# Kernel tuning notes

Hardware: AMD Instinct MI355X
Metric: run time of the kernel (lower is better)

Reference implementation:

```python
import jax, jax.numpy as jnp
import numpy as np

N_NODES = 200000
D = 128            # in_channels
B_GRAPHS = 512     # batch_size
STEPS = 3          # processing_steps


def setup_inputs() -> dict:
    key = jax.random.key(0)
    k = jax.random.split(key, 6)
    x = jax.random.normal(k[0], (N_NODES, D), dtype=jnp.float32)
    batch = jnp.sort(jax.random.randint(k[1], (N_NODES,), 0, B_GRAPHS, dtype=jnp.int64))
    s = 0.1
    W_ih = jax.random.normal(k[2], (3 * D, 2 * D), dtype=jnp.float32) * s
    W_hh = jax.random.normal(k[3], (3 * D, D), dtype=jnp.float32) * s
    b_ih = jax.random.normal(k[4], (3 * D,), dtype=jnp.float32) * s
    b_hh = jax.random.normal(k[5], (3 * D,), dtype=jnp.float32) * s
    return {"x": x, "batch": batch, "batch_size": B_GRAPHS,
            "W_ih": W_ih, "W_hh": W_hh, "b_ih": b_ih, "b_hh": b_hh}


def _gru_cell(inp, h, W_ih, W_hh, b_ih, b_hh):
    # inp: [B, 2d], h: [B, d]; PyTorch GRU gate order: r, z, n
    gi = inp @ W_ih.T + b_ih  # [B, 3d]
    gh = h @ W_hh.T + b_hh    # [B, 3d]
    gi_r, gi_z, gi_n = jnp.split(gi, 3, axis=-1)
    gh_r, gh_z, gh_n = jnp.split(gh, 3, axis=-1)
    r = jax.nn.sigmoid(gi_r + gh_r)
    z = jax.nn.sigmoid(gi_z + gh_z)
    n = jnp.tanh(gi_n + r * gh_n)
    return (1.0 - z) * n + z * h


def reference(x, batch, batch_size, W_ih, W_hh, b_ih, b_hh):
    B = batch_size
    d = x.shape[1]
    h = jnp.zeros((B, d), dtype=x.dtype)
    q_star = jnp.zeros((B, 2 * d), dtype=x.dtype)
    for _ in range(STEPS):
        h = _gru_cell(q_star, h, W_ih, W_hh, b_ih, b_hh)
        q = h  # num_layers=1: output == new hidden state
        e = jnp.sum(x * q[batch], axis=-1)  # [N]
        m = jax.ops.segment_max(e, batch, num_segments=B)
        ex = jnp.exp(e - m[batch])
        s = jax.ops.segment_sum(ex, batch, num_segments=B)
        a = ex / (s[batch] + 1e-16)  # segment softmax weights [N]
        r = jax.ops.segment_sum(a[:, None] * x, batch, num_segments=B)  # [B, d]
        q_star = jnp.concatenate([q, r], axis=-1)
    return q_star
```

## Files before the change

### kernel.cpp

```cpp
#include <hip/hip_runtime.h>
#include <math.h>

constexpr int D = 128;
constexpr int B = 512;
constexpr int STEPS = 3;
constexpr int NW_IH = 3 * D * 2 * D;
constexpr int NW_HH = 3 * D * D;

__device__ __forceinline__ float sigmoidf_(float x) { return 1.f / (1.f + __expf(-x)); }
__device__ __forceinline__ float bflo(unsigned int u) { return __uint_as_float(u << 16); }
__device__ __forceinline__ float bfhi(unsigned int u) { return __uint_as_float(u & 0xffff0000u); }
__device__ __forceinline__ unsigned short f2bf_rn(float f) {
    unsigned int u = __float_as_uint(f);
    u += 0x7fffu + ((u >> 16) & 1u);
    return (unsigned short)(u >> 16);
}

__global__ __launch_bounds__(256) void k_prep(const float* __restrict__ Wih,
        const float* __restrict__ Whh, const int* __restrict__ batch, int n,
        unsigned short* __restrict__ wih_bf, unsigned short* __restrict__ whh_bf,
        int* __restrict__ seg) {
    int i = blockIdx.x * blockDim.x + threadIdx.x;
    if (i < NW_IH) wih_bf[i] = f2bf_rn(Wih[i]);
    else if (i < NW_IH + NW_HH) whh_bf[i - NW_IH] = f2bf_rn(Whh[i - NW_IH]);
    if (i <= B) {
        int lo = 0, hi = n;
        while (lo < hi) { int mid = (lo + hi) >> 1; if (batch[mid] < i) lo = mid + 1; else hi = mid; }
        seg[i] = lo;
    }
}

__global__ __launch_bounds__(1024, 8) void k_set2set(
        const float* __restrict__ x,
        const unsigned short* __restrict__ wih_bf,
        const unsigned short* __restrict__ whh_bf,
        const float* __restrict__ bih, const float* __restrict__ bhh,
        const int* __restrict__ seg, float* __restrict__ out) {
    __shared__ __align__(16) float s_q[2 * D];
    __shared__ __align__(16) float s_h[D];
    __shared__ float s_gi[3 * D], s_gh[3 * D];
    __shared__ float sm[64], sl[64];
    __shared__ __align__(16) float rpart[16][D];

    const int b = blockIdx.x;
    const int tid = threadIdx.x;
    const int start = seg[b], end = seg[b + 1];
    const int g = tid >> 4;
    const int s = tid & 15;

    if (tid < 2 * D) s_q[tid] = 0.f;
    if (tid < D) s_h[tid] = 0.f;
    __syncthreads();

    for (int step = 0; step < STEPS; ++step) {
        if (tid < 768) {
            const int row  = tid >> 1;
            const int half = tid & 1;
            float gi = half ? 0.f : bih[row];
            float gh = half ? bhh[row] : 0.f;
            const float4* q4 = (const float4*)s_q;
            const float4* h4 = (const float4*)s_h;
            const uint4* wr = (const uint4*)(wih_bf + (size_t)row * (2 * D)) + half * 16;
#pragma unroll 4
            for (int c = 0; c < 16; ++c) {
                uint4 w = wr[c];
                float4 qa = q4[half * 32 + c * 2];
                float4 qb = q4[half * 32 + c * 2 + 1];
                gi = fmaf(bflo(w.x), qa.x, gi); gi = fmaf(bfhi(w.x), qa.y, gi);
                gi = fmaf(bflo(w.y), qa.z, gi); gi = fmaf(bfhi(w.y), qa.w, gi);
                gi = fmaf(bflo(w.z), qb.x, gi); gi = fmaf(bfhi(w.z), qb.y, gi);
                gi = fmaf(bflo(w.w), qb.z, gi); gi = fmaf(bfhi(w.w), qb.w, gi);
            }
            const uint4* vr = (const uint4*)(whh_bf + (size_t)row * D) + half * 8;
#pragma unroll 4
            for (int c = 0; c < 8; ++c) {
                uint4 w = vr[c];
                float4 ha = h4[half * 16 + c * 2];
                float4 hb = h4[half * 16 + c * 2 + 1];
                gh = fmaf(bflo(w.x), ha.x, gh); gh = fmaf(bfhi(w.x), ha.y, gh);
                gh = fmaf(bflo(w.y), ha.z, gh); gh = fmaf(bfhi(w.y), ha.w, gh);
                gh = fmaf(bflo(w.z), hb.x, gh); gh = fmaf(bfhi(w.z), hb.y, gh);
                gh = fmaf(bflo(w.w), hb.z, gh); gh = fmaf(bfhi(w.w), hb.w, gh);
            }
            gi += __shfl_xor(gi, 1, 64);
            gh += __shfl_xor(gh, 1, 64);
            if (!half) { s_gi[row] = gi; s_gh[row] = gh; }
        }
        __syncthreads();
        if (tid < D) {
            const int t = tid;
            float r  = sigmoidf_(s_gi[t] + s_gh[t]);
            float z  = sigmoidf_(s_gi[D + t] + s_gh[D + t]);
            float nn = tanhf(s_gi[2 * D + t] + r * s_gh[2 * D + t]);
            float hn = (1.f - z) * nn + z * s_h[t];
            s_h[t] = hn;
            s_q[t] = hn;
        }
        __syncthreads();

        const float4 q0 = ((const float4*)s_h)[s * 2];
        const float4 q1 = ((const float4*)s_h)[s * 2 + 1];
        float m_run = -INFINITY, l_run = 0.f;
        float4 acc0 = {0.f, 0.f, 0.f, 0.f};
        float4 acc1 = {0.f, 0.f, 0.f, 0.f};

        auto process = [&](const float4& v0, const float4& v1) {
            float p;
            p = v0.x * q0.x;
            p = fmaf(v0.y, q0.y, p); p = fmaf(v0.z, q0.z, p); p = fmaf(v0.w, q0.w, p);
            p = fmaf(v1.x, q1.x, p); p = fmaf(v1.y, q1.y, p);
            p = fmaf(v1.z, q1.z, p); p = fmaf(v1.w, q1.w, p);
            p += __shfl_xor(p, 1, 64);
            p += __shfl_xor(p, 2, 64);
            p += __shfl_xor(p, 4, 64);
            p += __shfl_xor(p, 8, 64);
            float nm = fmaxf(m_run, p);
            float sc = __expf(m_run - nm);
            float a  = __expf(p - nm);
            l_run = fmaf(l_run, sc, a);
            acc0.x = fmaf(acc0.x, sc, a * v0.x);
            acc0.y = fmaf(acc0.y, sc, a * v0.y);
            acc0.z = fmaf(acc0.z, sc, a * v0.z);
            acc0.w = fmaf(acc0.w, sc, a * v0.w);
            acc1.x = fmaf(acc1.x, sc, a * v1.x);
            acc1.y = fmaf(acc1.y, sc, a * v1.y);
            acc1.z = fmaf(acc1.z, sc, a * v1.z);
            acc1.w = fmaf(acc1.w, sc, a * v1.w);
            m_run = nm;
        };

        for (int n0 = start + g; n0 < end; n0 += 128) {
            const int n1 = n0 + 64;
            const float* p0 = x + (size_t)n0 * D + s * 8;
            float4 a0 = *(const float4*)p0;
            float4 a1 = *(const float4*)(p0 + 4);
            if (n1 < end) {
                const float* p1 = x + (size_t)n1 * D + s * 8;
                float4 b0 = *(const float4*)p1;
                float4 b1 = *(const float4*)(p1 + 4);
                process(a0, a1);
                process(b0, b1);
            } else {
                process(a0, a1);
            }
        }

        if (s == 0) { sm[g] = m_run; sl[g] = l_run; }
        __syncthreads();

        {
            const float mv = sm[tid & 63];
            const float lv = sl[tid & 63];
            float M = mv;
            M = fmaxf(M, __shfl_xor(M, 1, 64));
            M = fmaxf(M, __shfl_xor(M, 2, 64));
            M = fmaxf(M, __shfl_xor(M, 4, 64));
            M = fmaxf(M, __shfl_xor(M, 8, 64));
            M = fmaxf(M, __shfl_xor(M, 16, 64));
            M = fmaxf(M, __shfl_xor(M, 32, 64));
            float term = (mv == -INFINITY) ? 0.f : lv * __expf(mv - M);
            term += __shfl_xor(term, 1, 64);
            term += __shfl_xor(term, 2, 64);
            term += __shfl_xor(term, 4, 64);
            term += __shfl_xor(term, 8, 64);
            term += __shfl_xor(term, 16, 64);
            term += __shfl_xor(term, 32, 64);
            const float inv = 1.f / (term + 1e-16f);
            const float fac = (m_run == -INFINITY) ? 0.f : __expf(m_run - M) * inv;
            acc0.x *= fac; acc0.y *= fac; acc0.z *= fac; acc0.w *= fac;
            acc1.x *= fac; acc1.y *= fac; acc1.z *= fac; acc1.w *= fac;
        }
        acc0.x += __shfl_xor(acc0.x, 16, 64); acc0.y += __shfl_xor(acc0.y, 16, 64);
        acc0.z += __shfl_xor(acc0.z, 16, 64); acc0.w += __shfl_xor(acc0.w, 16, 64);
        acc1.x += __shfl_xor(acc1.x, 16, 64); acc1.y += __shfl_xor(acc1.y, 16, 64);
        acc1.z += __shfl_xor(acc1.z, 16, 64); acc1.w += __shfl_xor(acc1.w, 16, 64);
        acc0.x += __shfl_xor(acc0.x, 32, 64); acc0.y += __shfl_xor(acc0.y, 32, 64);
        acc0.z += __shfl_xor(acc0.z, 32, 64); acc0.w += __shfl_xor(acc0.w, 32, 64);
        acc1.x += __shfl_xor(acc1.x, 32, 64); acc1.y += __shfl_xor(acc1.y, 32, 64);
        acc1.z += __shfl_xor(acc1.z, 32, 64); acc1.w += __shfl_xor(acc1.w, 32, 64);

        const int wv = tid >> 6;
        if ((tid & 63) < 16) {
            float4* dst = (float4*)&rpart[wv][s * 8];
            dst[0] = acc0; dst[1] = acc1;
        }
        __syncthreads();
        if (tid < D) {
            float v = 0.f;
#pragma unroll
            for (int w = 0; w < 16; ++w) v += rpart[w][tid];
            s_q[D + tid] = v;
        }
        __syncthreads();
    }

    if (tid < 2 * D) out[(size_t)b * (2 * D) + tid] = s_q[tid];
}

extern "C" void kernel_launch(void* const* d_in, const int* in_sizes, int n_in,
                              void* d_out, int out_size, void* d_ws, size_t ws_size,
                              hipStream_t stream) {
    const float* x    = (const float*)d_in[0];
    const int*   batch= (const int*)d_in[1];
    const float* Wih  = (const float*)d_in[3];
    const float* Whh  = (const float*)d_in[4];
    const float* bih  = (const float*)d_in[5];
    const float* bhh  = (const float*)d_in[6];
    const int n = in_sizes[0] / D;

    char* ws = (char*)d_ws;
    int* seg = (int*)ws;
    unsigned short* wih_bf = (unsigned short*)(ws + 4096);
    unsigned short* whh_bf = (unsigned short*)(ws + 4096 + (size_t)NW_IH * 2);

    const int total = NW_IH + NW_HH;
    k_prep<<<(total + 255) / 256, 256, 0, stream>>>(Wih, Whh, batch, n, wih_bf, whh_bf, seg);
    k_set2set<<<B, 1024, 0, stream>>>(x, wih_bf, whh_bf, bih, bhh, seg, (float*)d_out);
}
```

Measured before the change: 259.5 us.

## Shrink set2set blocks to 256 threads with double-buffered 4-node batches

Cuts each graph's block from 1024 to 256 threads, so each 16-lane group handles four nodes per iteration. Node rows are loaded into register buffers one batch ahead, and the first batch is issued before the GRU matvec so the load overlaps it. The online softmax rescale is amortised across four nodes, and each GRU thread now computes two full rows with no shuffle. The cost is fewer threads per graph, more registers per thread, and a longer serial GRU phase per thread.

```diff
diff --git a/kernel.cpp b/kernel.cpp
--- a/kernel.cpp
+++ b/kernel.cpp
@@ -15,6 +15,7 @@
     u += 0x7fffu + ((u >> 16) & 1u);
     return (unsigned short)(u >> 16);
 }
+__device__ __forceinline__ float4 ld4(const float* p) { return *(const float4*)p; }
 
 __global__ __launch_bounds__(256) void k_prep(const float* __restrict__ Wih,
         const float* __restrict__ Whh, const int* __restrict__ batch, int n,
@@ -30,7 +31,9 @@
     }
 }
 
-__global__ __launch_bounds__(1024, 8) void k_set2set(
+struct Trip { float4 a0, a1, b0, b1, c0, c1, d0, d1; };
+
+__global__ __launch_bounds__(256, 2) void k_set2set(
         const float* __restrict__ x,
         const unsigned short* __restrict__ wih_bf,
         const unsigned short* __restrict__ whh_bf,
@@ -39,8 +42,8 @@
     __shared__ __align__(16) float s_q[2 * D];
     __shared__ __align__(16) float s_h[D];
     __shared__ float s_gi[3 * D], s_gh[3 * D];
-    __shared__ float sm[64], sl[64];
-    __shared__ __align__(16) float rpart[16][D];
+    __shared__ float sm[16], sl[16];
+    __shared__ __align__(16) float rpart[4][D];
 
     const int b = blockIdx.x;
     const int tid = threadIdx.x;
@@ -52,39 +55,120 @@
     if (tid < D) s_h[tid] = 0.f;
     __syncthreads();
 
+    const int len = end - start;
+    const int F = len >> 6;
+    const float* xb = x + (size_t)(start + g) * D + s * 8;
+
+    float m_run, l_run;
+    float4 acc0, acc1;
+    float4 q0, q1;
+
+    auto load_trip = [&](Trip& T, int t) {
+        const float* p = xb + (size_t)t * (64 * D);
+        T.a0 = ld4(p);            T.a1 = ld4(p + 4);
+        T.b0 = ld4(p + 16 * D);   T.b1 = ld4(p + 16 * D + 4);
+        T.c0 = ld4(p + 32 * D);   T.c1 = ld4(p + 32 * D + 4);
+        T.d0 = ld4(p + 48 * D);   T.d1 = ld4(p + 48 * D + 4);
+    };
+    auto dot8 = [&](const float4& lo, const float4& hi) {
+        float p = lo.x * q0.x;
+        p = fmaf(lo.y, q0.y, p); p = fmaf(lo.z, q0.z, p); p = fmaf(lo.w, q0.w, p);
+        p = fmaf(hi.x, q1.x, p); p = fmaf(hi.y, q1.y, p);
+        p = fmaf(hi.z, q1.z, p); p = fmaf(hi.w, q1.w, p);
+        return p;
+    };
+    auto compute = [&](const Trip& T) {
+        float p0 = dot8(T.a0, T.a1);
+        float p1 = dot8(T.b0, T.b1);
+        float p2 = dot8(T.c0, T.c1);
+        float p3 = dot8(T.d0, T.d1);
+        p0 += __shfl_xor(p0, 1, 64); p1 += __shfl_xor(p1, 1, 64);
+        p2 += __shfl_xor(p2, 1, 64); p3 += __shfl_xor(p3, 1, 64);
+        p0 += __shfl_xor(p0, 2, 64); p1 += __shfl_xor(p1, 2, 64);
+        p2 += __shfl_xor(p2, 2, 64); p3 += __shfl_xor(p3, 2, 64);
+        p0 += __shfl_xor(p0, 4, 64); p1 += __shfl_xor(p1, 4, 64);
+        p2 += __shfl_xor(p2, 4, 64); p3 += __shfl_xor(p3, 4, 64);
+        p0 += __shfl_xor(p0, 8, 64); p1 += __shfl_xor(p1, 8, 64);
+        p2 += __shfl_xor(p2, 8, 64); p3 += __shfl_xor(p3, 8, 64);
+        float nm = fmaxf(m_run, fmaxf(fmaxf(p0, p1), fmaxf(p2, p3)));
+        float sc = __expf(m_run - nm);
+        float e0 = __expf(p0 - nm), e1 = __expf(p1 - nm);
+        float e2 = __expf(p2 - nm), e3 = __expf(p3 - nm);
+        l_run = fmaf(l_run, sc, (e0 + e1) + (e2 + e3));
+        acc0.x = fmaf(acc0.x, sc, fmaf(e0, T.a0.x, fmaf(e1, T.b0.x, fmaf(e2, T.c0.x, e3 * T.d0.x))));
+        acc0.y = fmaf(acc0.y, sc, fmaf(e0, T.a0.y, fmaf(e1, T.b0.y, fmaf(e2, T.c0.y, e3 * T.d0.y))));
+        acc0.z = fmaf(acc0.z, sc, fmaf(e0, T.a0.z, fmaf(e1, T.b0.z, fmaf(e2, T.c0.z, e3 * T.d0.z))));
+        acc0.w = fmaf(acc0.w, sc, fmaf(e0, T.a0.w, fmaf(e1, T.b0.w, fmaf(e2, T.c0.w, e3 * T.d0.w))));
+        acc1.x = fmaf(acc1.x, sc, fmaf(e0, T.a1.x, fmaf(e1, T.b1.x, fmaf(e2, T.c1.x, e3 * T.d1.x))));
+        acc1.y = fmaf(acc1.y, sc, fmaf(e0, T.a1.y, fmaf(e1, T.b1.y, fmaf(e2, T.c1.y, e3 * T.d1.y))));
+        acc1.z = fmaf(acc1.z, sc, fmaf(e0, T.a1.z, fmaf(e1, T.b1.z, fmaf(e2, T.c1.z, e3 * T.d1.z))));
+        acc1.w = fmaf(acc1.w, sc, fmaf(e0, T.a1.w, fmaf(e1, T.b1.w, fmaf(e2, T.c1.w, e3 * T.d1.w))));
+        m_run = nm;
+    };
+    auto one_node = [&](const float4& v0, const float4& v1) {
+        float p = dot8(v0, v1);
+        p += __shfl_xor(p, 1, 64);
+        p += __shfl_xor(p, 2, 64);
+        p += __shfl_xor(p, 4, 64);
+        p += __shfl_xor(p, 8, 64);
+        float nm = fmaxf(m_run, p);
+        float sc = __expf(m_run - nm);
+        float e  = __expf(p - nm);
+        l_run = fmaf(l_run, sc, e);
+        acc0.x = fmaf(acc0.x, sc, e * v0.x);
+        acc0.y = fmaf(acc0.y, sc, e * v0.y);
+        acc0.z = fmaf(acc0.z, sc, e * v0.z);
+        acc0.w = fmaf(acc0.w, sc, e * v0.w);
+        acc1.x = fmaf(acc1.x, sc, e * v1.x);
+        acc1.y = fmaf(acc1.y, sc, e * v1.y);
+        acc1.z = fmaf(acc1.z, sc, e * v1.z);
+        acc1.w = fmaf(acc1.w, sc, e * v1.w);
+        m_run = nm;
+    };
+
+    Trip A, Bv;
+
     for (int step = 0; step < STEPS; ++step) {
-        if (tid < 768) {
-            const int row  = tid >> 1;
-            const int half = tid & 1;
-            float gi = half ? 0.f : bih[row];
-            float gh = half ? bhh[row] : 0.f;
+        if (F > 0) load_trip(A, 0);
+
+        if (tid < 192) {
+            const int r0 = tid * 2, r1 = r0 + 1;
+            float gi0 = bih[r0], gi1 = bih[r1];
+            float gh0 = bhh[r0], gh1 = bhh[r1];
             const float4* q4 = (const float4*)s_q;
             const float4* h4 = (const float4*)s_h;
-            const uint4* wr = (const uint4*)(wih_bf + (size_t)row * (2 * D)) + half * 16;
+            const uint4* w0 = (const uint4*)(wih_bf + (size_t)r0 * (2 * D));
+            const uint4* w1 = (const uint4*)(wih_bf + (size_t)r1 * (2 * D));
+#pragma unroll 4
+            for (int c = 0; c < 32; ++c) {
+                uint4 wa = w0[c], wb = w1[c];
+                float4 qa = q4[2 * c], qb = q4[2 * c + 1];
+                gi0 = fmaf(bflo(wa.x), qa.x, gi0); gi0 = fmaf(bfhi(wa.x), qa.y, gi0);
+                gi0 = fmaf(bflo(wa.y), qa.z, gi0); gi0 = fmaf(bfhi(wa.y), qa.w, gi0);
+                gi0 = fmaf(bflo(wa.z), qb.x, gi0); gi0 = fmaf(bfhi(wa.z), qb.y, gi0);
+                gi0 = fmaf(bflo(wa.w), qb.z, gi0); gi0 = fmaf(bfhi(wa.w), qb.w, gi0);
+                gi1 = fmaf(bflo(wb.x), qa.x, gi1); gi1 = fmaf(bfhi(wb.x), qa.y, gi1);
+                gi1 = fmaf(bflo(wb.y), qa.z, gi1); gi1 = fmaf(bfhi(wb.y), qa.w, gi1);
+                gi1 = fmaf(bflo(wb.z), qb.x, gi1); gi1 = fmaf(bfhi(wb.z), qb.y, gi1);
+                gi1 = fmaf(bflo(wb.w), qb.z, gi1); gi1 = fmaf(bfhi(wb.w), qb.w, gi1);
+            }
+            const uint4* v0 = (const uint4*)(whh_bf + (size_t)r0 * D);
+            const uint4* v1 = (const uint4*)(whh_bf + (size_t)r1 * D);
 #pragma unroll 4
             for (int c = 0; c < 16; ++c) {
-                uint4 w = wr[c];
-                float4 qa = q4[half * 32 + c * 2];
-                float4 qb = q4[half * 32 + c * 2 + 1];
-                gi = fmaf(bflo(w.x), qa.x, gi); gi = fmaf(bfhi(w.x), qa.y, gi);
-                gi = fmaf(bflo(w.y), qa.z, gi); gi = fmaf(bfhi(w.y), qa.w, gi);
-                gi = fmaf(bflo(w.z), qb.x, gi); gi = fmaf(bfhi(w.z), qb.y, gi);
-                gi = fmaf(bflo(w.w), qb.z, gi); gi = fmaf(bfhi(w.w), qb.w, gi);
-            }
-            const uint4* vr = (const uint4*)(whh_bf + (size_t)row * D) + half * 8;
-#pragma unroll 4
-            for (int c = 0; c < 8; ++c) {
-                uint4 w = vr[c];
-                float4 ha = h4[half * 16 + c * 2];
-                float4 hb = h4[half * 16 + c * 2 + 1];
-                gh = fmaf(bflo(w.x), ha.x, gh); gh = fmaf(bfhi(w.x), ha.y, gh);
-                gh = fmaf(bflo(w.y), ha.z, gh); gh = fmaf(bfhi(w.y), ha.w, gh);
-                gh = fmaf(bflo(w.z), hb.x, gh); gh = fmaf(bfhi(w.z), hb.y, gh);
-                gh = fmaf(bflo(w.w), hb.z, gh); gh = fmaf(bfhi(w.w), hb.w, gh);
-            }
-            gi += __shfl_xor(gi, 1, 64);
-            gh += __shfl_xor(gh, 1, 64);
-            if (!half) { s_gi[row] = gi; s_gh[row] = gh; }
+                uint4 wa = v0[c], wb = v1[c];
+                float4 ha = h4[2 * c], hb = h4[2 * c + 1];
+                gh0 = fmaf(bflo(wa.x), ha.x, gh0); gh0 = fmaf(bfhi(wa.x), ha.y, gh0);
+                gh0 = fmaf(bflo(wa.y), ha.z, gh0); gh0 = fmaf(bfhi(wa.y), ha.w, gh0);
+                gh0 = fmaf(bflo(wa.z), hb.x, gh0); gh0 = fmaf(bfhi(wa.z), hb.y, gh0);
+                gh0 = fmaf(bflo(wa.w), hb.z, gh0); gh0 = fmaf(bfhi(wa.w), hb.w, gh0);
+                gh1 = fmaf(bflo(wb.x), ha.x, gh1); gh1 = fmaf(bfhi(wb.x), ha.y, gh1);
+                gh1 = fmaf(bflo(wb.y), ha.z, gh1); gh1 = fmaf(bfhi(wb.y), ha.w, gh1);
+                gh1 = fmaf(bflo(wb.z), hb.x, gh1); gh1 = fmaf(bfhi(wb.z), hb.y, gh1);
+                gh1 = fmaf(bflo(wb.w), hb.z, gh1); gh1 = fmaf(bfhi(wb.w), hb.w, gh1);
+            }
+            s_gi[r0] = gi0; s_gi[r1] = gi1;
+            s_gh[r0] = gh0; s_gh[r1] = gh1;
         }
         __syncthreads();
         if (tid < D) {
@@ -98,50 +182,30 @@
         }
         __syncthreads();
 
-        const float4 q0 = ((const float4*)s_h)[s * 2];
-        const float4 q1 = ((const float4*)s_h)[s * 2 + 1];
-        float m_run = -INFINITY, l_run = 0.f;
-        float4 acc0 = {0.f, 0.f, 0.f, 0.f};
-        float4 acc1 = {0.f, 0.f, 0.f, 0.f};
-
-        auto process = [&](const float4& v0, const float4& v1) {
-            float p;
-            p = v0.x * q0.x;
-            p = fmaf(v0.y, q0.y, p); p = fmaf(v0.z, q0.z, p); p = fmaf(v0.w, q0.w, p);
-            p = fmaf(v1.x, q1.x, p); p = fmaf(v1.y, q1.y, p);
-            p = fmaf(v1.z, q1.z, p); p = fmaf(v1.w, q1.w, p);
-            p += __shfl_xor(p, 1, 64);
-            p += __shfl_xor(p, 2, 64);
-            p += __shfl_xor(p, 4, 64);
-            p += __shfl_xor(p, 8, 64);
-            float nm = fmaxf(m_run, p);
-            float sc = __expf(m_run - nm);
-            float a  = __expf(p - nm);
-            l_run = fmaf(l_run, sc, a);
-            acc0.x = fmaf(acc0.x, sc, a * v0.x);
-            acc0.y = fmaf(acc0.y, sc, a * v0.y);
-            acc0.z = fmaf(acc0.z, sc, a * v0.z);
-            acc0.w = fmaf(acc0.w, sc, a * v0.w);
-            acc1.x = fmaf(acc1.x, sc, a * v1.x);
-            acc1.y = fmaf(acc1.y, sc, a * v1.y);
-            acc1.z = fmaf(acc1.z, sc, a * v1.z);
-            acc1.w = fmaf(acc1.w, sc, a * v1.w);
-            m_run = nm;
-        };
-
-        for (int n0 = start + g; n0 < end; n0 += 128) {
-            const int n1 = n0 + 64;
-            const float* p0 = x + (size_t)n0 * D + s * 8;
-            float4 a0 = *(const float4*)p0;
-            float4 a1 = *(const float4*)(p0 + 4);
-            if (n1 < end) {
-                const float* p1 = x + (size_t)n1 * D + s * 8;
-                float4 b0 = *(const float4*)p1;
-                float4 b1 = *(const float4*)(p1 + 4);
-                process(a0, a1);
-                process(b0, b1);
-            } else {
-                process(a0, a1);
+        q0 = ((const float4*)s_h)[2 * s];
+        q1 = ((const float4*)s_h)[2 * s + 1];
+        m_run = -INFINITY; l_run = 0.f;
+        acc0 = make_float4(0.f, 0.f, 0.f, 0.f);
+        acc1 = make_float4(0.f, 0.f, 0.f, 0.f);
+
+        if (F > 0) {
+            int t = 0;
+            for (; t + 2 < F; t += 2) {
+                load_trip(Bv, t + 1); compute(A);
+                load_trip(A,  t + 2); compute(Bv);
+            }
+            if (t + 2 == F) { load_trip(Bv, t + 1); compute(A); compute(Bv); }
+            else            { compute(A); }
+        }
+        {
+            const int nt = start + g + (F << 6);
+#pragma unroll
+            for (int u = 0; u < 4; ++u) {
+                const int nd = nt + (u << 4);
+                if (nd < end) {
+                    const float* p = x + (size_t)nd * D + s * 8;
+                    one_node(ld4(p), ld4(p + 4));
+                }
             }
         }
 
@@ -149,22 +213,18 @@
         __syncthreads();
 
         {
-            const float mv = sm[tid & 63];
-            const float lv = sl[tid & 63];
+            const float mv = sm[s];
+            const float lv = sl[s];
             float M = mv;
             M = fmaxf(M, __shfl_xor(M, 1, 64));
             M = fmaxf(M, __shfl_xor(M, 2, 64));
             M = fmaxf(M, __shfl_xor(M, 4, 64));
             M = fmaxf(M, __shfl_xor(M, 8, 64));
-            M = fmaxf(M, __shfl_xor(M, 16, 64));
-            M = fmaxf(M, __shfl_xor(M, 32, 64));
             float term = (mv == -INFINITY) ? 0.f : lv * __expf(mv - M);
             term += __shfl_xor(term, 1, 64);
             term += __shfl_xor(term, 2, 64);
             term += __shfl_xor(term, 4, 64);
             term += __shfl_xor(term, 8, 64);
-            term += __shfl_xor(term, 16, 64);
-            term += __shfl_xor(term, 32, 64);
             const float inv = 1.f / (term + 1e-16f);
             const float fac = (m_run == -INFINITY) ? 0.f : __expf(m_run - M) * inv;
             acc0.x *= fac; acc0.y *= fac; acc0.z *= fac; acc0.w *= fac;
@@ -186,9 +246,7 @@
         }
         __syncthreads();
         if (tid < D) {
-            float v = 0.f;
-#pragma unroll
-            for (int w = 0; w < 16; ++w) v += rpart[w][tid];
+            float v = (rpart[0][tid] + rpart[1][tid]) + (rpart[2][tid] + rpart[3][tid]);
             s_q[D + tid] = v;
         }
         __syncthreads();
@@ -215,5 +273,5 @@
 
     const int total = NW_IH + NW_HH;
     k_prep<<<(total + 255) / 256, 256, 0, stream>>>(Wih, Whh, batch, n, wih_bf, whh_bf, seg);
-    k_set2set<<<B, 1024, 0, stream>>>(x, wih_bf, whh_bf, bih, bhh, seg, (float*)d_out);
-}
+    k_set2set<<<B, 256, 0, stream>>>(x, wih_bf, whh_bf, bih, bhh, seg, (float*)d_out);
+}
```

New measurement: 236.2 us. 9.0% less time.
